# Optimization experiments

Measured on AMD Instinct MI355X. Metric: run time of the kernel, lower is better.

Reference implementation:

```python
import jax, jax.numpy as jnp
import numpy as np
from jax import lax


def fps(xyz, npoint, init_far):
    # Faithful farthest-point sampling: sequential loop over npoint iterations.
    B, N, _ = xyz.shape
    bidx = jnp.arange(B)

    def step(carry, _):
        dist, far = carry
        c = xyz[bidx, far]                       # (B,3) current centroid
        d = jnp.sum((xyz - c[:, None, :]) ** 2, -1)  # (B,N)
        dist = jnp.minimum(dist, d)
        return (dist, jnp.argmax(dist, -1)), far     # emit index BEFORE update, as in torch

    init = (jnp.full((B, N), 1e10, xyz.dtype), init_far)
    _, cent = lax.scan(step, init, None, length=npoint)  # (npoint, B)
    return cent.T                                         # (B, npoint)


def gather_pts(feat, idx):
    # feat (B,N,C), idx (B,K) -> (B,K,C)
    return jnp.take_along_axis(feat, idx[..., None], axis=1)


def setup_inputs() -> dict:
    key = jax.random.key(0)
    ks = jax.random.split(key, 12)
    B, N = 128, 500

    def w(k, o, i):
        return jax.random.normal(k, (o, i), jnp.float32) * 0.02

    z = lambda o: jnp.zeros((o,), jnp.float32)
    return {
        "x": jax.random.normal(ks[0], (B, N, 3), jnp.float32),
        "conf_W": w(ks[1], 1, 3),   "conf_b": z(1),
        "w1": w(ks[2], 64, 4),      "b1": z(64),
        "w2": w(ks[3], 256, 64),    "b2": z(256),
        "pc1_W": w(ks[4], 256, 256),"pc1_b": z(256),
        "w3": w(ks[5], 256, 259),   "b3": z(256),
        "w4": w(ks[6], 384, 256),   "b4": z(384),
        "pc2_W": w(ks[7], 384, 384),"pc2_b": z(384),
        "w5": w(ks[8], 384, 387),   "b5": z(384),
        "w6": w(ks[9], 512, 384),   "b6": z(512),
        "model_weights": 0,
        "init_far1": jax.random.randint(ks[10], (B,), 0, N),
        "init_far2": jax.random.randint(ks[11], (B,), 0, N),
    }


def reference(x, conf_W, conf_b, w1, b1, w2, b2, pc1_W, pc1_b,
              w3, b3, w4, b4, pc2_W, pc2_b, w5, b5, w6, b6,
              model_weights, init_far1, init_far2):
    relu = jax.nn.relu
    lin = lambda h, W, b: h @ W.T + b

    # ConfidenceScorePredictor: per-point sigmoid score (1 channel)
    conf = jax.nn.sigmoid(lin(x, conf_W, conf_b))            # (B,N,1)
    feat = jnp.concatenate([conf, x], -1)                    # (B,N,4)

    l2 = relu(lin(relu(lin(feat, w1, b1)), w2, b2))          # (B,N,256)
    l3 = lin(l2, pc1_W, pc1_b)                               # Conv1d k=1 == per-point linear

    idx1 = fps(x, 500, init_far1)                            # (B,500)
    nf1 = jnp.concatenate([gather_pts(l3, idx1), gather_pts(x, idx1)], -1)  # (B,500,259)

    l5 = relu(lin(relu(lin(nf1, w3, b3)), w4, b4))           # (B,500,384)
    l6 = lin(l5, pc2_W, pc2_b)                               # (B,500,384)

    idx2 = fps(x, 1000, init_far2)                           # (B,1000), indices < 500
    nf2 = jnp.concatenate([gather_pts(l6, idx2), gather_pts(x, idx2)], -1)  # (B,1000,387)

    l8 = relu(lin(relu(lin(nf2, w5, b5)), w6, b6))           # (B,1000,512)
    return jnp.max(l8, axis=1)                               # MaxPool1d(k=1000) -> (B,512)
```

## Files before the change

### kernel.cpp

```cpp
#include <hip/hip_runtime.h>

typedef unsigned short u16;
typedef short bf16x8 __attribute__((ext_vector_type(8)));
typedef float f32x4 __attribute__((ext_vector_type(4)));
typedef unsigned short us8 __attribute__((ext_vector_type(8)));
typedef unsigned long long u64;

__device__ __forceinline__ float bf2f(u16 u) {
  return __uint_as_float(((unsigned)u) << 16);
}
__device__ __forceinline__ u16 f2bf(float f) {
  unsigned u = __float_as_uint(f);
  u += 0x7fffu + ((u >> 16) & 1u);
  return (u16)(u >> 16);
}
__device__ __forceinline__ float rlf(float v, int l) {
  return __uint_as_float((unsigned)__builtin_amdgcn_readlane(__float_as_int(v), l));
}
__device__ __forceinline__ void gload16(const u16* g, u16* l) {
  __builtin_amdgcn_global_load_lds(
      (const __attribute__((address_space(1))) void*)g,
      (__attribute__((address_space(3))) void*)l, 16, 0, 0);
}

#define M_AB 64000
#define M_C 65536

#define OFF_ARENA_B 49152000u
#define OFF_IDX1 149815296u
#define OFF_FPSD 150071296u
#define OFF_FPSI 150333440u
#define OFF_WB   150583296u

template <int CTRL>
__device__ __forceinline__ float dppmaxf(float v) {
  int s = __builtin_amdgcn_update_dpp(0, __float_as_int(v), CTRL, 0xF, 0xF, true);
  return fmaxf(v, __uint_as_float((unsigned)s));
}

__device__ void fps_seg(const float4* cpt, int* out, const int* init1,
                        float* dstate, int* fstate, int b, int t0, int tcnt,
                        int lane) {
  float px[8], py[8], pz[8], dist[8];
  int base = lane * 8;
#pragma unroll
  for (int j = 0; j < 8; ++j) {
    int p = base + j;
    float4 c = cpt[p < 500 ? p : 0];
    px[j] = c.x; py[j] = c.y; pz[j] = c.z;
  }
  int fidx;
  if (t0 == 0) {
#pragma unroll
    for (int j = 0; j < 8; ++j) dist[j] = 1e10f;
    fidx = init1[b];
  } else {
#pragma unroll
    for (int j = 0; j < 8; ++j) dist[j] = dstate[(b * 64 + lane) * 8 + j];
    fidx = fstate[b];
  }
  float4 c0 = cpt[fidx];
  float cx = c0.x, cy = c0.y, cz = c0.z;

  int tend = t0 + tcnt;
  for (int t = t0; t < tend; ++t) {
    if (lane == 0) out[t] = fidx;
    if (t == 499) return;
#pragma unroll
    for (int j = 0; j < 8; ++j) {
      float dx = __fsub_rn(px[j], cx);
      float dy = __fsub_rn(py[j], cy);
      float dz = __fsub_rn(pz[j], cz);
      float d = __fadd_rn(__fadd_rn(__fmul_rn(dx, dx), __fmul_rn(dy, dy)),
                          __fmul_rn(dz, dz));
      dist[j] = fminf(dist[j], d);
    }
    float m01 = fmaxf(dist[0], dist[1]), m23 = fmaxf(dist[2], dist[3]);
    float m45 = fmaxf(dist[4], dist[5]), m67 = fmaxf(dist[6], dist[7]);
    float lm = fmaxf(fmaxf(m01, m23), fmaxf(m45, m67));
    lm = dppmaxf<0x111>(lm);
    lm = dppmaxf<0x112>(lm);
    lm = dppmaxf<0x114>(lm);
    lm = dppmaxf<0x118>(lm);
    lm = dppmaxf<0x142>(lm);
    lm = dppmaxf<0x143>(lm);
    float mf = rlf(lm, 63);
    int sel = 8;
    float sx = 0.f, sy = 0.f, sz = 0.f;
#pragma unroll
    for (int j = 7; j >= 0; --j) {
      bool hit = (dist[j] == mf);
      sel = hit ? j : sel;
      sx = hit ? px[j] : sx;
      sy = hit ? py[j] : sy;
      sz = hit ? pz[j] : sz;
    }
    u64 mask = __ballot(sel != 8);
    int li = (int)__ffsll(mask) - 1;
    fidx = li * 8 + __builtin_amdgcn_readlane(sel, li);
    cx = rlf(sx, li);
    cy = rlf(sy, li);
    cz = rlf(sz, li);
  }
#pragma unroll
  for (int j = 0; j < 8; ++j) dstate[(b * 64 + lane) * 8 + j] = dist[j];
  if (lane == 0) fstate[b] = fidx;
}

#define SMEM_BYTES (16384 * 2 + 1024)

__device__ __forceinline__ void gemm_body(
    const u16* __restrict__ A, int lda, const float* __restrict__ X,
    const int* __restrict__ idx, int mode, const u16* __restrict__ Wb,
    int ldw, const float* __restrict__ bias, u16* __restrict__ C, int ldc,
    int Kp, int N, int act, float* __restrict__ outf, int bx, int by,
    char* smem, int t) {
  u16* lA = (u16*)smem;
  u16* lB = (u16*)(smem + 16384);
  float* red = (float*)(smem + 32768);

  const int m0 = bx * 128, n0 = by * 128;
  const int w = t >> 6, lane = t & 63;
  const int mrow = lane & 15, quad = lane >> 4;
  const int wm = w >> 1, wn = w & 1;

  const int lrow8 = lane >> 3;
  const int sseg = (lane & 7) ^ lrow8;

  const u16* arow[4];
  const u16* wrow[4];
#pragma unroll
  for (int i = 0; i < 4; ++i) {
    int gr = m0 + w * 32 + i * 8 + lrow8;
    if (mode == 4) {
      int b = gr >> 9;
      int p = gr & 511;
      int pe = (p < 500) ? p : 0;
      int s = idx[b * 500 + pe];
      arow[i] = A + ((size_t)b * 500 + s) * lda;
    } else {
      arow[i] = A + (size_t)gr * lda;
    }
    wrow[i] = Wb + (size_t)(n0 + w * 32 + i * 8 + lrow8) * ldw;
  }
  const int fr = t >> 1;
  const int fs0 = (t & 1) * 4;
  const u16* faptr;
  const float* fxptr = nullptr;
  {
    int gr = m0 + fr;
    if (mode == 4) {
      int b = gr >> 9;
      int p = gr & 511;
      int pe = (p < 500) ? p : 0;
      int s = idx[b * 500 + pe];
      faptr = A + ((size_t)b * 500 + s) * lda;
      fxptr = X + ((size_t)b * 500 + pe) * 3;
    } else {
      faptr = A + (size_t)gr * lda;
      if (mode == 2) fxptr = X + (size_t)gr * 3;
    }
  }
  const int kfull = lda & ~63;

  f32x4 acc[4][4];
  const f32x4 fz = {0.f, 0.f, 0.f, 0.f};
#pragma unroll
  for (int i = 0; i < 4; ++i)
#pragma unroll
    for (int j = 0; j < 4; ++j) acc[i][j] = fz;

  for (int k0 = 0; k0 < Kp; k0 += 64) {
    __syncthreads();
#pragma unroll
    for (int i = 0; i < 4; ++i)
      gload16(wrow[i] + k0 + sseg * 8, lB + (w * 32 + i * 8) * 64);
    if (k0 < kfull) {
#pragma unroll
      for (int i = 0; i < 4; ++i)
        gload16(arow[i] + k0 + sseg * 8, lA + (w * 32 + i * 8) * 64);
    } else {
#pragma unroll
      for (int s4 = 0; s4 < 4; ++s4) {
        int seg = fs0 + s4;
        us8 v = {0, 0, 0, 0, 0, 0, 0, 0};
        int kb = k0 + seg * 8;
#pragma unroll
        for (int j = 0; j < 8; ++j) {
          int k = kb + j;
          u16 vv = 0;
          if (k < lda) vv = faptr[k];
          else if (mode != 0 && k < lda + 3) vv = f2bf(fxptr[k - lda]);
          v[j] = vv;
        }
        *(us8*)(lA + fr * 64 + (seg ^ (fr & 7)) * 8) = v;
      }
    }
    __syncthreads();

#pragma unroll
    for (int kh = 0; kh < 2; ++kh) {
      bf16x8 af[4], bfv[4];
#pragma unroll
      for (int mi = 0; mi < 4; ++mi) {
        int r = wm * 64 + mi * 16 + mrow;
        af[mi] = *(const bf16x8*)(lA + r * 64 + ((kh * 4 + quad) ^ (r & 7)) * 8);
      }
#pragma unroll
      for (int ni = 0; ni < 4; ++ni) {
        int r = wn * 64 + ni * 16 + mrow;
        bfv[ni] = *(const bf16x8*)(lB + r * 64 + ((kh * 4 + quad) ^ (r & 7)) * 8);
      }
#pragma unroll
      for (int mi = 0; mi < 4; ++mi)
#pragma unroll
        for (int ni = 0; ni < 4; ++ni)
          acc[mi][ni] = __builtin_amdgcn_mfma_f32_16x16x32_bf16(
              af[mi], bfv[ni], acc[mi][ni], 0, 0, 0);
    }
  }

  if (act < 2) {
#pragma unroll
    for (int ni = 0; ni < 4; ++ni) {
      int col = n0 + wn * 64 + ni * 16 + mrow;
      if (col >= N) continue;
      float bv = bias[col];
#pragma unroll
      for (int mi = 0; mi < 4; ++mi)
#pragma unroll
        for (int r = 0; r < 4; ++r) {
          int grow = m0 + wm * 64 + mi * 16 + quad * 4 + r;
          float v = acc[mi][ni][r] + bv;
          if (act == 1) v = fmaxf(v, 0.f);
          C[(size_t)grow * ldc + col] = f2bf(v);
        }
    }
  } else {
#pragma unroll
    for (int ni = 0; ni < 4; ++ni) {
      int col = n0 + wn * 64 + ni * 16 + mrow;
      float bv = (col < N) ? bias[col] : 0.f;
      float mx = 0.f;
#pragma unroll
      for (int mi = 0; mi < 4; ++mi)
#pragma unroll
        for (int r = 0; r < 4; ++r) {
          int grow = m0 + wm * 64 + mi * 16 + quad * 4 + r;
          float v = fmaxf(acc[mi][ni][r] + bv, 0.f);
          if ((grow & 511) < 500) mx = fmaxf(mx, v);
        }
      mx = fmaxf(mx, __shfl_xor(mx, 16, 64));
      mx = fmaxf(mx, __shfl_xor(mx, 32, 64));
      if (quad == 0) red[wm * 128 + wn * 64 + ni * 16 + mrow] = mx;
    }
    __syncthreads();
    if (t < 128) {
      int col = n0 + t;
      if (col < N) {
        float m = fmaxf(red[t], red[128 + t]);
        int b = m0 >> 9;
        atomicMax((unsigned*)&outf[b * 512 + col], __float_as_uint(m));
      }
    }
  }
}

__global__ __launch_bounds__(256) void gemm_mfma(
    const u16* __restrict__ A, int lda, const float* __restrict__ X,
    const int* __restrict__ idx, int mode, const u16* __restrict__ Wb,
    int ldw, const float* __restrict__ bias, u16* __restrict__ C, int ldc,
    int Kp, int N, int act, float* __restrict__ outf) {
  __shared__ __align__(16) char smem[SMEM_BYTES];
  gemm_body(A, lda, X, idx, mode, Wb, ldw, bias, C, ldc, Kp, N, act, outf,
            blockIdx.x, blockIdx.y, smem, threadIdx.x);
}

__global__ __launch_bounds__(256) void gemm_fps(
    const u16* __restrict__ A, int lda, const float* __restrict__ X,
    int mode, const u16* __restrict__ Wb, int ldw,
    const float* __restrict__ bias, u16* __restrict__ C, int ldc, int Kp,
    int N, int act, int gx, const float* __restrict__ x,
    const int* __restrict__ init1, int* __restrict__ idx1,
    float* __restrict__ dstate, int* __restrict__ fstate, int t0, int tcnt) {
  __shared__ __align__(16) char smem[SMEM_BYTES];
  int bid = blockIdx.x;
  int t = threadIdx.x;
  if (bid < 128) {
    int b = bid;
    float4* cpt = (float4*)smem;
    const float* xb = x + (size_t)b * 1500;
    for (int p = t; p < 500; p += 256)
      cpt[p] = make_float4(xb[p * 3], xb[p * 3 + 1], xb[p * 3 + 2], 0.f);
    __syncthreads();
    if (t < 64)
      fps_seg(cpt, idx1 + b * 500, init1, dstate, fstate, b, t0, tcnt, t);
  } else {
    int g = bid - 128;
    int by = g / gx, bx = g - by * gx;
    gemm_body(A, lda, X, nullptr, mode, Wb, ldw, bias, C, ldc, Kp, N, act,
              nullptr, bx, by, smem, t);
  }
}

struct PrepArgs {
  const float* wsrc[8];
  u16* wdst[8];
  int wN[8], wK[8], wKp[8];
  int wstart[9];
};

__global__ __launch_bounds__(256) void prep_kernel(
    PrepArgs pa, const float* __restrict__ x, const float* __restrict__ cW,
    const float* __restrict__ cb, u16* __restrict__ feat,
    float* __restrict__ outf, const int* __restrict__ init1,
    int* __restrict__ idx1, float* __restrict__ dstate,
    int* __restrict__ fstate, int tcnt) {
  __shared__ float4 cpt[512];
  int bid = blockIdx.x;
  int t = threadIdx.x;
  if (bid < 128) {
    int b = bid;
    const float* xb = x + (size_t)b * 1500;
    for (int p = t; p < 500; p += 256)
      cpt[p] = make_float4(xb[p * 3], xb[p * 3 + 1], xb[p * 3 + 2], 0.f);
    __syncthreads();
    if (t < 64) fps_seg(cpt, idx1 + b * 500, init1, dstate, fstate, b, 0, tcnt, t);
    return;
  }
  int i = (bid - 128) * 256 + t;
  int S = pa.wstart[8];
  if (i < S) {
    int w = 0;
#pragma unroll
    for (int j = 1; j < 8; ++j)
      if (i >= pa.wstart[j]) w = j;
    int local = i - pa.wstart[w];
    int Kp = pa.wKp[w];
    int n = local / Kp, k = local - n * Kp;
    pa.wdst[w][local] =
        (n < pa.wN[w] && k < pa.wK[w]) ? f2bf(pa.wsrc[w][n * pa.wK[w] + k]) : (u16)0;
  } else if (i < S + 65536) {
    outf[i - S] = 0.f;
  } else {
    int r = i - S - 65536;
    if (r < M_AB) {
      float x0 = x[r * 3], x1 = x[r * 3 + 1], x2 = x[r * 3 + 2];
      float z = x0 * cW[0] + x1 * cW[1] + x2 * cW[2] + cb[0];
      float conf = 1.0f / (1.0f + expf(-z));
      feat[r * 4 + 0] = f2bf(conf);
      feat[r * 4 + 1] = f2bf(x0);
      feat[r * 4 + 2] = f2bf(x1);
      feat[r * 4 + 3] = f2bf(x2);
    }
  }
}

extern "C" void kernel_launch(void* const* d_in, const int* in_sizes, int n_in,
                              void* d_out, int out_size, void* d_ws,
                              size_t ws_size, hipStream_t stream) {
  const float* x      = (const float*)d_in[0];
  const float* conf_W = (const float*)d_in[1];
  const float* conf_b = (const float*)d_in[2];
  const float* w1     = (const float*)d_in[3];
  const float* b1     = (const float*)d_in[4];
  const float* w2     = (const float*)d_in[5];
  const float* b2     = (const float*)d_in[6];
  const float* pc1_W  = (const float*)d_in[7];
  const float* pc1_b  = (const float*)d_in[8];
  const float* w3     = (const float*)d_in[9];
  const float* b3     = (const float*)d_in[10];
  const float* w4     = (const float*)d_in[11];
  const float* b4     = (const float*)d_in[12];
  const float* pc2_W  = (const float*)d_in[13];
  const float* pc2_b  = (const float*)d_in[14];
  const float* w5     = (const float*)d_in[15];
  const float* b5     = (const float*)d_in[16];
  const float* w6     = (const float*)d_in[17];
  const float* b6     = (const float*)d_in[18];
  const int* init1    = (const int*)d_in[20];

  char* ws = (char*)d_ws;
  u16* feat = (u16*)(ws + 0);
  u16* l2b  = (u16*)(ws + 0);
  u16* l4b  = (u16*)(ws + 0);
  u16* l6u  = (u16*)(ws + 0);
  u16* l1b  = (u16*)(ws + OFF_ARENA_B);
  u16* l3b  = (u16*)(ws + OFF_ARENA_B);
  u16* l5b  = (u16*)(ws + OFF_ARENA_B);
  u16* l7b  = (u16*)(ws + OFF_ARENA_B);
  int* idx1 = (int*)(ws + OFF_IDX1);
  float* dstate = (float*)(ws + OFF_FPSD);
  int* fstate   = (int*)(ws + OFF_FPSI);
  u16* wb   = (u16*)(ws + OFF_WB);
  float* outf = (float*)d_out;

  PrepArgs pa;
  const float* srcs[8] = {w1, w2, pc1_W, w3, w4, pc2_W, w5, w6};
  int Ns[8]  = {64, 256, 256, 256, 384, 384, 384, 512};
  int Nps[8] = {128, 256, 256, 256, 384, 384, 384, 512};
  int Ks[8]  = {4, 64, 256, 259, 256, 384, 387, 384};
  int Kps[8] = {64, 64, 256, 320, 256, 384, 448, 384};
  u16* WBp[8];
  int cum = 0;
  for (int i = 0; i < 8; ++i) {
    pa.wsrc[i] = srcs[i];
    pa.wdst[i] = WBp[i] = wb + cum;
    pa.wN[i] = Ns[i];
    pa.wK[i] = Ks[i];
    pa.wKp[i] = Kps[i];
    pa.wstart[i] = cum;
    cum += Nps[i] * Kps[i];
  }
  pa.wstart[8] = cum;
  int total = cum + 65536 + M_AB;

  prep_kernel<<<128 + (total + 255) / 256, 256, 0, stream>>>(
      pa, x, conf_W, conf_b, feat, outf, init1, idx1, dstate, fstate, 60);
  gemm_fps<<<128 + 500, 256, 0, stream>>>(feat, 4, nullptr, 0, WBp[0], 64,
      b1, l1b, 64, 64, 64, 1, 500, x, init1, idx1, dstate, fstate, 60, 40);
  gemm_fps<<<128 + 1000, 256, 0, stream>>>(l1b, 64, nullptr, 0, WBp[1], 64,
      b2, l2b, 256, 64, 256, 1, 500, x, init1, idx1, dstate, fstate, 100, 50);
  gemm_fps<<<128 + 1000, 256, 0, stream>>>(l2b, 256, nullptr, 0, WBp[2], 256,
      pc1_b, l3b, 256, 256, 256, 0, 500, x, init1, idx1, dstate, fstate, 150, 70);
  gemm_fps<<<128 + 1000, 256, 0, stream>>>(l3b, 256, x, 2, WBp[3], 320,
      b3, l4b, 256, 320, 256, 1, 500, x, init1, idx1, dstate, fstate, 220, 85);
  gemm_fps<<<128 + 1500, 256, 0, stream>>>(l4b, 256, nullptr, 0, WBp[4], 256,
      b4, l5b, 384, 256, 384, 1, 500, x, init1, idx1, dstate, fstate, 305, 90);
  gemm_fps<<<128 + 1500, 256, 0, stream>>>(l5b, 384, nullptr, 0, WBp[5], 384,
      pc2_b, l6u, 384, 384, 384, 0, 500, x, init1, idx1, dstate, fstate, 395, 105);
  gemm_mfma<<<dim3(512, 3), 256, 0, stream>>>(l6u, 384, x, idx1, 4,
      WBp[6], 448, b5, l7b, 384, 448, 384, 1, nullptr);
  gemm_mfma<<<dim3(512, 4), 256, 0, stream>>>(l7b, 384, nullptr, nullptr, 0,
      WBp[7], 384, b6, nullptr, 0, 384, 512, 2, outf);
}
```

Measured before the change: 395.4 us.

## Fuse MLP chain into two persistent kernels with LDS-resident activations

Replaces the eight separate GEMM launches with two fused kernels. The first computes the confidence score and the first four per-point layers in LDS on 96-row tiles, writes the l5/l6 outputs to global memory, and runs the remaining FPS iterations in the same launch. The second gathers l6 rows by FPS index, runs w5 and then w6 with a fused max-pool, and reads B operands straight from global memory instead of staging them in LDS. This removes intermediate global round trips and launch overhead, at the cost of higher register and LDS pressure and uncached direct weight loads.

```diff
diff --git a/kernel.cpp b/kernel.cpp
--- a/kernel.cpp
+++ b/kernel.cpp
@@ -6,9 +6,6 @@
 typedef unsigned short us8 __attribute__((ext_vector_type(8)));
 typedef unsigned long long u64;
 
-__device__ __forceinline__ float bf2f(u16 u) {
-  return __uint_as_float(((unsigned)u) << 16);
-}
 __device__ __forceinline__ u16 f2bf(float f) {
   unsigned u = __float_as_uint(f);
   u += 0x7fffu + ((u >> 16) & 1u);
@@ -17,20 +14,14 @@
 __device__ __forceinline__ float rlf(float v, int l) {
   return __uint_as_float((unsigned)__builtin_amdgcn_readlane(__float_as_int(v), l));
 }
-__device__ __forceinline__ void gload16(const u16* g, u16* l) {
-  __builtin_amdgcn_global_load_lds(
-      (const __attribute__((address_space(1))) void*)g,
-      (__attribute__((address_space(3))) void*)l, 16, 0, 0);
-}
-
-#define M_AB 64000
-#define M_C 65536
-
-#define OFF_ARENA_B 49152000u
-#define OFF_IDX1 149815296u
-#define OFF_FPSD 150071296u
-#define OFF_FPSI 150333440u
-#define OFF_WB   150583296u
+
+#define OFF_L5S 0u
+#define OFF_L6U 49152000u
+#define OFF_L7S 98304000u
+#define OFF_IDX1 148635648u
+#define OFF_FPSD 148891648u
+#define OFF_FPSI 149153792u
+#define OFF_WB   149154304u
 
 template <int CTRL>
 __device__ __forceinline__ float dppmaxf(float v) {
@@ -107,199 +98,300 @@
   if (lane == 0) fstate[b] = fidx;
 }
 
-#define SMEM_BYTES (16384 * 2 + 1024)
-
-__device__ __forceinline__ void gemm_body(
-    const u16* __restrict__ A, int lda, const float* __restrict__ X,
-    const int* __restrict__ idx, int mode, const u16* __restrict__ Wb,
-    int ldw, const float* __restrict__ bias, u16* __restrict__ C, int ldc,
-    int Kp, int N, int act, float* __restrict__ outf, int bx, int by,
-    char* smem, int t) {
-  u16* lA = (u16*)smem;
-  u16* lB = (u16*)(smem + 16384);
-  float* red = (float*)(smem + 32768);
-
-  const int m0 = bx * 128, n0 = by * 128;
-  const int w = t >> 6, lane = t & 63;
-  const int mrow = lane & 15, quad = lane >> 4;
-  const int wm = w >> 1, wn = w & 1;
-
-  const int lrow8 = lane >> 3;
-  const int sseg = (lane & 7) ^ lrow8;
-
-  const u16* arow[4];
-  const u16* wrow[4];
-#pragma unroll
-  for (int i = 0; i < 4; ++i) {
-    int gr = m0 + w * 32 + i * 8 + lrow8;
-    if (mode == 4) {
-      int b = gr >> 9;
-      int p = gr & 511;
-      int pe = (p < 500) ? p : 0;
-      int s = idx[b * 500 + pe];
-      arow[i] = A + ((size_t)b * 500 + s) * lda;
-    } else {
-      arow[i] = A + (size_t)gr * lda;
-    }
-    wrow[i] = Wb + (size_t)(n0 + w * 32 + i * 8 + lrow8) * ldw;
-  }
-  const int fr = t >> 1;
-  const int fs0 = (t & 1) * 4;
-  const u16* faptr;
-  const float* fxptr = nullptr;
-  {
-    int gr = m0 + fr;
-    if (mode == 4) {
-      int b = gr >> 9;
-      int p = gr & 511;
-      int pe = (p < 500) ? p : 0;
-      int s = idx[b * 500 + pe];
-      faptr = A + ((size_t)b * 500 + s) * lda;
-      fxptr = X + ((size_t)b * 500 + pe) * 3;
-    } else {
-      faptr = A + (size_t)gr * lda;
-      if (mode == 2) fxptr = X + (size_t)gr * 3;
-    }
-  }
-  const int kfull = lda & ~63;
-
-  f32x4 acc[4][4];
-  const f32x4 fz = {0.f, 0.f, 0.f, 0.f};
-#pragma unroll
-  for (int i = 0; i < 4; ++i)
-#pragma unroll
-    for (int j = 0; j < 4; ++j) acc[i][j] = fz;
-
-  for (int k0 = 0; k0 < Kp; k0 += 64) {
-    __syncthreads();
-#pragma unroll
-    for (int i = 0; i < 4; ++i)
-      gload16(wrow[i] + k0 + sseg * 8, lB + (w * 32 + i * 8) * 64);
-    if (k0 < kfull) {
-#pragma unroll
-      for (int i = 0; i < 4; ++i)
-        gload16(arow[i] + k0 + sseg * 8, lA + (w * 32 + i * 8) * 64);
-    } else {
-#pragma unroll
-      for (int s4 = 0; s4 < 4; ++s4) {
-        int seg = fs0 + s4;
-        us8 v = {0, 0, 0, 0, 0, 0, 0, 0};
-        int kb = k0 + seg * 8;
-#pragma unroll
-        for (int j = 0; j < 8; ++j) {
-          int k = kb + j;
-          u16 vv = 0;
-          if (k < lda) vv = faptr[k];
-          else if (mode != 0 && k < lda + 3) vv = f2bf(fxptr[k - lda]);
-          v[j] = vv;
+template <int MI, int NI, int NP, int AG, int XC>
+__device__ __forceinline__ void gemm_acc(
+    f32x4 acc[MI][NI], const u16* __restrict__ aL, int Win, int smask,
+    int arow0, const u16* const* aG, const u16* __restrict__ xc,
+    const u16* __restrict__ bb, int Kp, int mrow, int quad) {
+#pragma unroll
+  for (int mi = 0; mi < MI; ++mi)
+#pragma unroll
+    for (int ni = 0; ni < NI; ++ni) acc[mi][ni] = f32x4{0.f, 0.f, 0.f, 0.f};
+#pragma unroll
+  for (int kp = 0; kp < NP + XC; ++kp) {
+    bf16x8 af[MI];
+#pragma unroll
+    for (int mi = 0; mi < MI; ++mi) {
+      int r = arow0 + mi * 16 + mrow;
+      if (XC && kp == NP)
+        af[mi] = *(const bf16x8*)(xc + r * 32 + ((quad ^ (r & 3)) << 3));
+      else if (AG)
+        af[mi] = *(const bf16x8*)(aG[mi] + kp * 32);
+      else
+        af[mi] = *(const bf16x8*)(aL + r * Win +
+                                  (((kp * 4 + quad) ^ (r & smask)) << 3));
+    }
+    bf16x8 bf[NI];
+#pragma unroll
+    for (int ni = 0; ni < NI; ++ni)
+      bf[ni] = *(const bf16x8*)(bb + (size_t)ni * 16 * Kp + kp * 32);
+#pragma unroll
+    for (int mi = 0; mi < MI; ++mi)
+#pragma unroll
+      for (int ni = 0; ni < NI; ++ni)
+        acc[mi][ni] = __builtin_amdgcn_mfma_f32_16x16x32_bf16(
+            af[mi], bf[ni], acc[mi][ni], 0, 0, 0);
+  }
+}
+
+template <int MI, int NI>
+__device__ __forceinline__ void ep_lds(const f32x4 acc[MI][NI], u16* out,
+                                       int Wout, const float* __restrict__ bias,
+                                       int n0, int arow0, int relu, int mrow,
+                                       int quad) {
+#pragma unroll
+  for (int ni = 0; ni < NI; ++ni) {
+    int col = n0 + ni * 16 + mrow;
+    float bv = bias[col];
+    int seg0 = col >> 3, lo = col & 7;
+#pragma unroll
+    for (int mi = 0; mi < MI; ++mi)
+#pragma unroll
+      for (int r = 0; r < 4; ++r) {
+        int row = arow0 + mi * 16 + quad * 4 + r;
+        float v = acc[mi][ni][r] + bv;
+        if (relu) v = fmaxf(v, 0.f);
+        out[row * Wout + ((seg0 ^ (row & 7)) << 3) + lo] = f2bf(v);
+      }
+  }
+}
+
+template <int MI, int NI>
+__device__ __forceinline__ void ep_glb(const f32x4 acc[MI][NI],
+                                       u16* __restrict__ out, int ldo,
+                                       const float* __restrict__ bias, int n0,
+                                       long grow0, long rowlim, int relu,
+                                       int mrow, int quad) {
+#pragma unroll
+  for (int ni = 0; ni < NI; ++ni) {
+    int col = n0 + ni * 16 + mrow;
+    float bv = bias[col];
+#pragma unroll
+    for (int mi = 0; mi < MI; ++mi)
+#pragma unroll
+      for (int r = 0; r < 4; ++r) {
+        long grow = grow0 + mi * 16 + quad * 4 + r;
+        if (grow < rowlim) {
+          float v = acc[mi][ni][r] + bv;
+          if (relu) v = fmaxf(v, 0.f);
+          out[(size_t)grow * ldo + col] = f2bf(v);
         }
-        *(us8*)(lA + fr * 64 + (seg ^ (fr & 7)) * 8) = v;
       }
-    }
-    __syncthreads();
-
-#pragma unroll
-    for (int kh = 0; kh < 2; ++kh) {
-      bf16x8 af[4], bfv[4];
-#pragma unroll
-      for (int mi = 0; mi < 4; ++mi) {
-        int r = wm * 64 + mi * 16 + mrow;
-        af[mi] = *(const bf16x8*)(lA + r * 64 + ((kh * 4 + quad) ^ (r & 7)) * 8);
-      }
-#pragma unroll
-      for (int ni = 0; ni < 4; ++ni) {
-        int r = wn * 64 + ni * 16 + mrow;
-        bfv[ni] = *(const bf16x8*)(lB + r * 64 + ((kh * 4 + quad) ^ (r & 7)) * 8);
-      }
-#pragma unroll
-      for (int mi = 0; mi < 4; ++mi)
-#pragma unroll
-        for (int ni = 0; ni < 4; ++ni)
-          acc[mi][ni] = __builtin_amdgcn_mfma_f32_16x16x32_bf16(
-              af[mi], bfv[ni], acc[mi][ni], 0, 0, 0);
-    }
-  }
-
-  if (act < 2) {
-#pragma unroll
-    for (int ni = 0; ni < 4; ++ni) {
-      int col = n0 + wn * 64 + ni * 16 + mrow;
-      if (col >= N) continue;
-      float bv = bias[col];
-#pragma unroll
-      for (int mi = 0; mi < 4; ++mi)
-#pragma unroll
-        for (int r = 0; r < 4; ++r) {
-          int grow = m0 + wm * 64 + mi * 16 + quad * 4 + r;
-          float v = acc[mi][ni][r] + bv;
-          if (act == 1) v = fmaxf(v, 0.f);
-          C[(size_t)grow * ldc + col] = f2bf(v);
-        }
-    }
-  } else {
-#pragma unroll
-    for (int ni = 0; ni < 4; ++ni) {
-      int col = n0 + wn * 64 + ni * 16 + mrow;
-      float bv = (col < N) ? bias[col] : 0.f;
-      float mx = 0.f;
-#pragma unroll
-      for (int mi = 0; mi < 4; ++mi)
-#pragma unroll
-        for (int r = 0; r < 4; ++r) {
-          int grow = m0 + wm * 64 + mi * 16 + quad * 4 + r;
-          float v = fmaxf(acc[mi][ni][r] + bv, 0.f);
-          if ((grow & 511) < 500) mx = fmaxf(mx, v);
-        }
-      mx = fmaxf(mx, __shfl_xor(mx, 16, 64));
-      mx = fmaxf(mx, __shfl_xor(mx, 32, 64));
-      if (quad == 0) red[wm * 128 + wn * 64 + ni * 16 + mrow] = mx;
-    }
-    __syncthreads();
-    if (t < 128) {
-      int col = n0 + t;
-      if (col < N) {
-        float m = fmaxf(red[t], red[128 + t]);
-        int b = m0 >> 9;
-        atomicMax((unsigned*)&outf[b * 512 + col], __float_as_uint(m));
-      }
-    }
-  }
-}
-
-__global__ __launch_bounds__(256) void gemm_mfma(
-    const u16* __restrict__ A, int lda, const float* __restrict__ X,
-    const int* __restrict__ idx, int mode, const u16* __restrict__ Wb,
-    int ldw, const float* __restrict__ bias, u16* __restrict__ C, int ldc,
-    int Kp, int N, int act, float* __restrict__ outf) {
-  __shared__ __align__(16) char smem[SMEM_BYTES];
-  gemm_body(A, lda, X, idx, mode, Wb, ldw, bias, C, ldc, Kp, N, act, outf,
-            blockIdx.x, blockIdx.y, smem, threadIdx.x);
-}
-
-__global__ __launch_bounds__(256) void gemm_fps(
-    const u16* __restrict__ A, int lda, const float* __restrict__ X,
-    int mode, const u16* __restrict__ Wb, int ldw,
-    const float* __restrict__ bias, u16* __restrict__ C, int ldc, int Kp,
-    int N, int act, int gx, const float* __restrict__ x,
+  }
+}
+
+struct ABArgs {
+  const u16 *w1, *w2, *pc1, *w3, *w4, *pc2;
+  const float *b1, *b2, *pc1b, *b3, *b4, *pc2b;
+};
+
+__global__ __launch_bounds__(512, 4) void fused_ab(
+    ABArgs A, const float* __restrict__ x, const float* __restrict__ cW,
+    const float* __restrict__ cb, u16* __restrict__ l5s, u16* __restrict__ l6u,
     const int* __restrict__ init1, int* __restrict__ idx1,
     float* __restrict__ dstate, int* __restrict__ fstate, int t0, int tcnt) {
-  __shared__ __align__(16) char smem[SMEM_BYTES];
-  int bid = blockIdx.x;
-  int t = threadIdx.x;
+  __shared__ __align__(16) u16 act[96 * 256];
+  __shared__ __align__(16) u16 xcat[96 * 32];
+  int bid = blockIdx.x, t = threadIdx.x;
   if (bid < 128) {
-    int b = bid;
-    float4* cpt = (float4*)smem;
-    const float* xb = x + (size_t)b * 1500;
-    for (int p = t; p < 500; p += 256)
+    float4* cpt = (float4*)act;
+    const float* xb = x + (size_t)bid * 1500;
+    for (int p = t; p < 500; p += 512)
       cpt[p] = make_float4(xb[p * 3], xb[p * 3 + 1], xb[p * 3 + 2], 0.f);
     __syncthreads();
     if (t < 64)
-      fps_seg(cpt, idx1 + b * 500, init1, dstate, fstate, b, t0, tcnt, t);
-  } else {
-    int g = bid - 128;
-    int by = g / gx, bx = g - by * gx;
-    gemm_body(A, lda, X, nullptr, mode, Wb, ldw, bias, C, ldc, Kp, N, act,
-              nullptr, bx, by, smem, t);
+      fps_seg(cpt, idx1 + bid * 500, init1, dstate, fstate, bid, t0, tcnt, t);
+    return;
+  }
+  const int blk = bid - 128;
+  const size_t rows0 = (size_t)blk * 96;
+  if (t < 96) {
+    size_t gr = rows0 + t;
+    if (gr > 63999) gr = 63999;
+    float x0 = x[gr * 3], x1 = x[gr * 3 + 1], x2 = x[gr * 3 + 2];
+    float z = x0 * cW[0] + x1 * cW[1] + x2 * cW[2] + cb[0];
+    float conf = 1.0f / (1.0f + expf(-z));
+    us8 fv;
+    fv[0] = f2bf(conf); fv[1] = f2bf(x0); fv[2] = f2bf(x1); fv[3] = f2bf(x2);
+    fv[4] = 0; fv[5] = 0; fv[6] = 0; fv[7] = 0;
+    *(us8*)(act + t * 32 + ((t & 3) << 3)) = fv;
+    us8 xv;
+    xv[0] = fv[1]; xv[1] = fv[2]; xv[2] = fv[3];
+    xv[3] = 0; xv[4] = 0; xv[5] = 0; xv[6] = 0; xv[7] = 0;
+    *(us8*)(xcat + t * 32 + ((t & 3) << 3)) = xv;
+  }
+  if (t < 288) {
+    us8 zz = {0, 0, 0, 0, 0, 0, 0, 0};
+    int r = t / 3, s = 1 + t % 3;
+    *(us8*)(act + r * 32 + ((s ^ (r & 3)) << 3)) = zz;
+    *(us8*)(xcat + r * 32 + ((s ^ (r & 3)) << 3)) = zz;
+  }
+  __syncthreads();
+  const int w = t >> 6, lane = t & 63, mrow = lane & 15, quad = lane >> 4;
+  const int wm = w >> 2, wn = w & 3;
+  const int arow0 = wm * 48;
+  {
+    f32x4 acc[3][1];
+    const u16* bb = A.w1 + (size_t)(wn * 16 + mrow) * 32 + quad * 8;
+    gemm_acc<3, 1, 1, 0, 0>(acc, act, 32, 3, arow0, nullptr, nullptr, bb, 32,
+                            mrow, quad);
+    __syncthreads();
+    ep_lds<3, 1>(acc, act, 64, A.b1, wn * 16, arow0, 1, mrow, quad);
+    __syncthreads();
+  }
+  {
+    f32x4 acc[3][4];
+    const u16* bb = A.w2 + (size_t)(wn * 64 + mrow) * 64 + quad * 8;
+    gemm_acc<3, 4, 2, 0, 0>(acc, act, 64, 7, arow0, nullptr, nullptr, bb, 64,
+                            mrow, quad);
+    __syncthreads();
+    ep_lds<3, 4>(acc, act, 256, A.b2, wn * 64, arow0, 1, mrow, quad);
+    __syncthreads();
+  }
+  {
+    f32x4 acc[3][4];
+    const u16* bb = A.pc1 + (size_t)(wn * 64 + mrow) * 256 + quad * 8;
+    gemm_acc<3, 4, 8, 0, 0>(acc, act, 256, 7, arow0, nullptr, nullptr, bb, 256,
+                            mrow, quad);
+    __syncthreads();
+    ep_lds<3, 4>(acc, act, 256, A.pc1b, wn * 64, arow0, 0, mrow, quad);
+    __syncthreads();
+  }
+  {
+    f32x4 acc[3][4];
+    const u16* bb = A.w3 + (size_t)(wn * 64 + mrow) * 288 + quad * 8;
+    gemm_acc<3, 4, 8, 0, 1>(acc, act, 256, 7, arow0, nullptr, xcat, bb, 288,
+                            mrow, quad);
+    __syncthreads();
+    ep_lds<3, 4>(acc, act, 256, A.b3, wn * 64, arow0, 1, mrow, quad);
+    __syncthreads();
+  }
+#pragma unroll
+  for (int ph = 0; ph < 2; ++ph) {
+    f32x4 acc[3][3];
+    int n0 = ph * 192 + wn * 48;
+    const u16* bb = A.w4 + (size_t)(n0 + mrow) * 256 + quad * 8;
+    gemm_acc<3, 3, 8, 0, 0>(acc, act, 256, 7, arow0, nullptr, nullptr, bb, 256,
+                            mrow, quad);
+    ep_glb<3, 3>(acc, l5s, 384, A.b4, n0, (long)(rows0 + arow0), 64000, 1,
+                 mrow, quad);
+  }
+  __threadfence_block();
+  __syncthreads();
+  {
+    const u16* aG[3];
+#pragma unroll
+    for (int mi = 0; mi < 3; ++mi) {
+      size_t r = rows0 + arow0 + mi * 16 + mrow;
+      if (r > 63999) r = 63999;
+      aG[mi] = l5s + r * 384 + quad * 8;
+    }
+#pragma unroll
+    for (int ph = 0; ph < 2; ++ph) {
+      f32x4 acc[3][3];
+      int n0 = ph * 192 + wn * 48;
+      const u16* bb = A.pc2 + (size_t)(n0 + mrow) * 384 + quad * 8;
+      gemm_acc<3, 3, 12, 1, 0>(acc, nullptr, 0, 0, arow0, aG, nullptr, bb, 384,
+                               mrow, quad);
+      ep_glb<3, 3>(acc, l6u, 384, A.pc2b, n0, (long)(rows0 + arow0), 64000, 0,
+                   mrow, quad);
+    }
+  }
+}
+
+struct CArgs {
+  const u16 *w5, *w6;
+  const float *b5, *b6;
+};
+
+__global__ __launch_bounds__(512, 4) void fused_c(
+    CArgs C, const float* __restrict__ x, const u16* __restrict__ l6u,
+    u16* __restrict__ l7s, float* __restrict__ outf,
+    const int* __restrict__ idx1) {
+  __shared__ __align__(16) u16 xcat[128 * 32];
+  __shared__ float red[2][256];
+  int bid = blockIdx.x, t = threadIdx.x;
+  const int b = bid >> 2, q = bid & 3;
+  const int prow0 = q * 128;
+  if (t < 128) {
+    int p = prow0 + t, pe = p < 500 ? p : 0;
+    const float* xp = x + ((size_t)b * 500 + pe) * 3;
+    us8 xv;
+    xv[0] = f2bf(xp[0]); xv[1] = f2bf(xp[1]); xv[2] = f2bf(xp[2]);
+    xv[3] = 0; xv[4] = 0; xv[5] = 0; xv[6] = 0; xv[7] = 0;
+    *(us8*)(xcat + t * 32 + ((t & 3) << 3)) = xv;
+  }
+  if (t < 384) {
+    us8 zz = {0, 0, 0, 0, 0, 0, 0, 0};
+    int r = t / 3, s = 1 + t % 3;
+    *(us8*)(xcat + r * 32 + ((s ^ (r & 3)) << 3)) = zz;
+  }
+  __syncthreads();
+  const int w = t >> 6, lane = t & 63, mrow = lane & 15, quad = lane >> 4;
+  const int wm = w >> 2, wn = w & 3;
+  const int arow0 = wm * 64;
+  const size_t grow0 = (size_t)b * 512 + prow0 + arow0;
+  {
+    const u16* aG[4];
+#pragma unroll
+    for (int mi = 0; mi < 4; ++mi) {
+      int p = prow0 + arow0 + mi * 16 + mrow;
+      int pe = p < 500 ? p : 0;
+      int s = idx1[b * 500 + pe];
+      aG[mi] = l6u + ((size_t)b * 500 + s) * 384 + quad * 8;
+    }
+#pragma unroll
+    for (int ph = 0; ph < 2; ++ph) {
+      f32x4 acc[4][3];
+      int n0 = ph * 192 + wn * 48;
+      const u16* bb = C.w5 + (size_t)(n0 + mrow) * 416 + quad * 8;
+      gemm_acc<4, 3, 12, 1, 1>(acc, nullptr, 0, 0, arow0, aG, xcat, bb, 416,
+                               mrow, quad);
+      ep_glb<4, 3>(acc, l7s, 384, C.b5, n0, (long)grow0, 1L << 30, 1, mrow,
+                   quad);
+    }
+  }
+  __threadfence_block();
+  __syncthreads();
+  {
+    const u16* aG[4];
+#pragma unroll
+    for (int mi = 0; mi < 4; ++mi) {
+      size_t r = grow0 + mi * 16 + mrow;
+      aG[mi] = l7s + r * 384 + quad * 8;
+    }
+#pragma unroll
+    for (int ph = 0; ph < 2; ++ph) {
+      f32x4 acc[4][4];
+      int n0 = ph * 256 + wn * 64;
+      const u16* bb = C.w6 + (size_t)(n0 + mrow) * 384 + quad * 8;
+      gemm_acc<4, 4, 12, 1, 0>(acc, nullptr, 0, 0, arow0, aG, nullptr, bb, 384,
+                               mrow, quad);
+#pragma unroll
+      for (int ni = 0; ni < 4; ++ni) {
+        int cc = n0 + ni * 16 + mrow;
+        float bv = C.b6[cc];
+        float mx = 0.f;
+#pragma unroll
+        for (int mi = 0; mi < 4; ++mi)
+#pragma unroll
+          for (int r = 0; r < 4; ++r) {
+            int p = prow0 + arow0 + mi * 16 + quad * 4 + r;
+            float v = fmaxf(acc[mi][ni][r] + bv, 0.f);
+            if (p < 500) mx = fmaxf(mx, v);
+          }
+        mx = fmaxf(mx, __shfl_xor(mx, 16, 64));
+        mx = fmaxf(mx, __shfl_xor(mx, 32, 64));
+        if (quad == 0) red[wm][wn * 64 + ni * 16 + mrow] = mx;
+      }
+      __syncthreads();
+      if (t < 256) {
+        float m = fmaxf(red[0][t], red[1][t]);
+        atomicMax((unsigned*)&outf[(size_t)b * 512 + ph * 256 + t],
+                  __float_as_uint(m));
+      }
+      __syncthreads();
+    }
   }
 }
 
@@ -311,48 +403,34 @@
 };
 
 __global__ __launch_bounds__(256) void prep_kernel(
-    PrepArgs pa, const float* __restrict__ x, const float* __restrict__ cW,
-    const float* __restrict__ cb, u16* __restrict__ feat,
-    float* __restrict__ outf, const int* __restrict__ init1,
-    int* __restrict__ idx1, float* __restrict__ dstate,
-    int* __restrict__ fstate, int tcnt) {
+    PrepArgs pa, const float* __restrict__ x, float* __restrict__ outf,
+    const int* __restrict__ init1, int* __restrict__ idx1,
+    float* __restrict__ dstate, int* __restrict__ fstate, int tcnt) {
   __shared__ float4 cpt[512];
-  int bid = blockIdx.x;
-  int t = threadIdx.x;
+  int bid = blockIdx.x, t = threadIdx.x;
   if (bid < 128) {
-    int b = bid;
-    const float* xb = x + (size_t)b * 1500;
+    const float* xb = x + (size_t)bid * 1500;
     for (int p = t; p < 500; p += 256)
       cpt[p] = make_float4(xb[p * 3], xb[p * 3 + 1], xb[p * 3 + 2], 0.f);
     __syncthreads();
-    if (t < 64) fps_seg(cpt, idx1 + b * 500, init1, dstate, fstate, b, 0, tcnt, t);
+    if (t < 64)
+      fps_seg(cpt, idx1 + bid * 500, init1, dstate, fstate, bid, 0, tcnt, t);
     return;
   }
   int i = (bid - 128) * 256 + t;
   int S = pa.wstart[8];
   if (i < S) {
-    int w = 0;
+    int wsel = 0;
 #pragma unroll
     for (int j = 1; j < 8; ++j)
-      if (i >= pa.wstart[j]) w = j;
-    int local = i - pa.wstart[w];
-    int Kp = pa.wKp[w];
+      if (i >= pa.wstart[j]) wsel = j;
+    int local = i - pa.wstart[wsel];
+    int Kp = pa.wKp[wsel];
     int n = local / Kp, k = local - n * Kp;
-    pa.wdst[w][local] =
-        (n < pa.wN[w] && k < pa.wK[w]) ? f2bf(pa.wsrc[w][n * pa.wK[w] + k]) : (u16)0;
+    pa.wdst[wsel][local] =
+        (k < pa.wK[wsel]) ? f2bf(pa.wsrc[wsel][n * pa.wK[wsel] + k]) : (u16)0;
   } else if (i < S + 65536) {
     outf[i - S] = 0.f;
-  } else {
-    int r = i - S - 65536;
-    if (r < M_AB) {
-      float x0 = x[r * 3], x1 = x[r * 3 + 1], x2 = x[r * 3 + 2];
-      float z = x0 * cW[0] + x1 * cW[1] + x2 * cW[2] + cb[0];
-      float conf = 1.0f / (1.0f + expf(-z));
-      feat[r * 4 + 0] = f2bf(conf);
-      feat[r * 4 + 1] = f2bf(x0);
-      feat[r * 4 + 2] = f2bf(x1);
-      feat[r * 4 + 3] = f2bf(x2);
-    }
   }
 }
 
@@ -381,26 +459,20 @@
   const int* init1    = (const int*)d_in[20];
 
   char* ws = (char*)d_ws;
-  u16* feat = (u16*)(ws + 0);
-  u16* l2b  = (u16*)(ws + 0);
-  u16* l4b  = (u16*)(ws + 0);
-  u16* l6u  = (u16*)(ws + 0);
-  u16* l1b  = (u16*)(ws + OFF_ARENA_B);
-  u16* l3b  = (u16*)(ws + OFF_ARENA_B);
-  u16* l5b  = (u16*)(ws + OFF_ARENA_B);
-  u16* l7b  = (u16*)(ws + OFF_ARENA_B);
+  u16* l5s = (u16*)(ws + OFF_L5S);
+  u16* l6u = (u16*)(ws + OFF_L6U);
+  u16* l7s = (u16*)(ws + OFF_L7S);
   int* idx1 = (int*)(ws + OFF_IDX1);
   float* dstate = (float*)(ws + OFF_FPSD);
-  int* fstate   = (int*)(ws + OFF_FPSI);
-  u16* wb   = (u16*)(ws + OFF_WB);
+  int* fstate = (int*)(ws + OFF_FPSI);
+  u16* wb = (u16*)(ws + OFF_WB);
   float* outf = (float*)d_out;
 
   PrepArgs pa;
   const float* srcs[8] = {w1, w2, pc1_W, w3, w4, pc2_W, w5, w6};
   int Ns[8]  = {64, 256, 256, 256, 384, 384, 384, 512};
-  int Nps[8] = {128, 256, 256, 256, 384, 384, 384, 512};
   int Ks[8]  = {4, 64, 256, 259, 256, 384, 387, 384};
-  int Kps[8] = {64, 64, 256, 320, 256, 384, 448, 384};
+  int Kps[8] = {32, 64, 256, 288, 256, 384, 416, 384};
   u16* WBp[8];
   int cum = 0;
   for (int i = 0; i < 8; ++i) {
@@ -410,27 +482,22 @@
     pa.wK[i] = Ks[i];
     pa.wKp[i] = Kps[i];
     pa.wstart[i] = cum;
-    cum += Nps[i] * Kps[i];
+    cum += Ns[i] * Kps[i];
   }
   pa.wstart[8] = cum;
-  int total = cum + 65536 + M_AB;
+  int total = cum + 65536;
 
   prep_kernel<<<128 + (total + 255) / 256, 256, 0, stream>>>(
-      pa, x, conf_W, conf_b, feat, outf, init1, idx1, dstate, fstate, 60);
-  gemm_fps<<<128 + 500, 256, 0, stream>>>(feat, 4, nullptr, 0, WBp[0], 64,
-      b1, l1b, 64, 64, 64, 1, 500, x, init1, idx1, dstate, fstate, 60, 40);
-  gemm_fps<<<128 + 1000, 256, 0, stream>>>(l1b, 64, nullptr, 0, WBp[1], 64,
-      b2, l2b, 256, 64, 256, 1, 500, x, init1, idx1, dstate, fstate, 100, 50);
-  gemm_fps<<<128 + 1000, 256, 0, stream>>>(l2b, 256, nullptr, 0, WBp[2], 256,
-      pc1_b, l3b, 256, 256, 256, 0, 500, x, init1, idx1, dstate, fstate, 150, 70);
-  gemm_fps<<<128 + 1000, 256, 0, stream>>>(l3b, 256, x, 2, WBp[3], 320,
-      b3, l4b, 256, 320, 256, 1, 500, x, init1, idx1, dstate, fstate, 220, 85);
-  gemm_fps<<<128 + 1500, 256, 0, stream>>>(l4b, 256, nullptr, 0, WBp[4], 256,
-      b4, l5b, 384, 256, 384, 1, 500, x, init1, idx1, dstate, fstate, 305, 90);
-  gemm_fps<<<128 + 1500, 256, 0, stream>>>(l5b, 384, nullptr, 0, WBp[5], 384,
-      pc2_b, l6u, 384, 384, 384, 0, 500, x, init1, idx1, dstate, fstate, 395, 105);
-  gemm_mfma<<<dim3(512, 3), 256, 0, stream>>>(l6u, 384, x, idx1, 4,
-      WBp[6], 448, b5, l7b, 384, 448, 384, 1, nullptr);
-  gemm_mfma<<<dim3(512, 4), 256, 0, stream>>>(l7b, 384, nullptr, nullptr, 0,
-      WBp[7], 384, b6, nullptr, 0, 384, 512, 2, outf);
-}
+      pa, x, outf, init1, idx1, dstate, fstate, 64);
+
+  ABArgs A;
+  A.w1 = WBp[0]; A.w2 = WBp[1]; A.pc1 = WBp[2];
+  A.w3 = WBp[3]; A.w4 = WBp[4]; A.pc2 = WBp[5];
+  A.b1 = b1; A.b2 = b2; A.pc1b = pc1_b; A.b3 = b3; A.b4 = b4; A.pc2b = pc2_b;
+  fused_ab<<<128 + 667, 512, 0, stream>>>(A, x, conf_W, conf_b, l5s, l6u,
+                                          init1, idx1, dstate, fstate, 64, 436);
+
+  CArgs Cg;
+  Cg.w5 = WBp[6]; Cg.w6 = WBp[7]; Cg.b5 = b5; Cg.b6 = b6;
+  fused_c<<<512, 512, 0, stream>>>(Cg, x, l6u, l7s, outf, idx1);
+}
```

Measured after the change: 644.0 us. +62.9%, slower.
